# Optimization experiments

Hardware: AMD Instinct MI355X
Metric: run time of the kernel (lower is better)

## Reference

```python
import jax, jax.numpy as jnp
import numpy as np

B, L, D = 8, 4096, 1024
MAX_CHUNKS = 128
BOUNDARY_P = 0.03  # ~123 boundaries per sequence, just under max_chunks


def setup_inputs() -> dict:
    key = jax.random.key(0)
    kx, kb = jax.random.split(key)
    x = jax.random.normal(kx, (B, L, D), dtype=jnp.float32)
    # float 'boundary probabilities'; forward thresholds at 0.5 -> produce 0/1 floats
    boundaries = (jax.random.uniform(kb, (B, L)) < BOUNDARY_P).astype(jnp.float32)
    return {"x": x, "boundaries": boundaries}


def reference(x, boundaries):
    """Vectorized equivalent of ChunkLayer.forward.

    Chunk i of a sequence spans [b_i, b_{i+1}) for consecutive boundary
    positions (last chunk runs to seq end). Tokens before the first
    boundary get segment id -1 and are dropped, matching the torch loop.
    Output is mean-pooled chunks, zero-padded/truncated to MAX_CHUNKS.
    """
    Bb, Ll, Dd = x.shape
    bmask = (boundaries > 0.5).astype(jnp.int32)          # [B, L]
    seg = jnp.cumsum(bmask, axis=1) - 1                   # [B, L], -1 before first boundary
    # route dropped (seg<0) and overflow (seg>=MAX_CHUNKS) tokens to a trash segment
    seg = jnp.where((seg < 0) | (seg >= MAX_CHUNKS), MAX_CHUNKS, seg)

    def per_batch(xi, si):
        sums = jax.ops.segment_sum(xi, si, num_segments=MAX_CHUNKS + 1)[:MAX_CHUNKS]       # [C, D]
        cnts = jax.ops.segment_sum(jnp.ones((Ll,), xi.dtype), si,
                                   num_segments=MAX_CHUNKS + 1)[:MAX_CHUNKS]               # [C]
        return sums, cnts

    sums, cnts = jax.vmap(per_batch)(x, seg)              # [B, C, D], [B, C]
    means = jnp.where(cnts[..., None] > 0,
                      sums / jnp.maximum(cnts, 1.0)[..., None],
                      0.0)                                # zero-pad empty chunks
    return means, cnts.astype(jnp.int32)
```

## Files before the change

kernel.cpp:

```cpp
#include <hip/hip_runtime.h>

#define B_DIM 8
#define L_DIM 4096
#define D_DIM 1024
#define MAXC 128
#define RG 4
#define CT 256

__device__ __forceinline__ void f4add(float4& a, const float4& v) {
    a.x += v.x; a.y += v.y; a.z += v.z; a.w += v.w;
}

__global__ __launch_bounds__(1024, 8)
void fused_chunk_kernel(const float* __restrict__ x,
                        const float* __restrict__ bnd,
                        float* __restrict__ out_means,
                        float* __restrict__ out_cnts)
{
    const int bc   = blockIdx.x;
    const int b    = bc >> 7;
    const int c    = bc & (MAXC - 1);
    const int t    = threadIdx.x;
    const int tc   = t & (CT - 1);
    const int rg   = t >> 8;
    const int lane = t & 63;
    const int w    = t >> 6;

    __shared__ int wtot[16];
    __shared__ int sb[2];
    __shared__ float4 red[RG][CT];

    if (t == 0) { sb[0] = 0; sb[1] = L_DIM; }

    const float4 bv = reinterpret_cast<const float4*>(bnd + (size_t)b * L_DIM)[t];
    unsigned m = 0u;
    if (bv.x > 0.5f) m |= 1u;
    if (bv.y > 0.5f) m |= 2u;
    if (bv.z > 0.5f) m |= 4u;
    if (bv.w > 0.5f) m |= 8u;
    const int cnt4 = __popc(m);

    int incl = cnt4;
#pragma unroll
    for (int off = 1; off < 64; off <<= 1) {
        int u = __shfl_up(incl, off, 64);
        if (lane >= off) incl += u;
    }
    if (lane == 63) wtot[w] = incl;
    __syncthreads();

    int waveoff = 0, n = 0;
#pragma unroll
    for (int i = 0; i < 16; ++i) {
        const int ww = wtot[i];
        n += ww;
        if (i < w) waveoff += ww;
    }

    if (m != 0u) {
        int idx = waveoff + incl - cnt4;
        const int base = t * 4;
#pragma unroll
        for (int j = 0; j < 4; ++j) {
            if (m & (1u << j)) {
                if (idx == c)     sb[0] = base + j;
                if (idx == c + 1) sb[1] = base + j;
                ++idx;
            }
        }
    }
    __syncthreads();

    int cnt = 0;
    float4 a0 = make_float4(0.f, 0.f, 0.f, 0.f);
    float4 a1 = a0, a2 = a0, a3 = a0;

    if (c < n) {
        const int start = sb[0];
        const int end   = sb[1];
        cnt = end - start;

        const int nr = (cnt - rg + RG - 1) / RG;
        const float* xp = x + ((size_t)b * L_DIM + start + rg) * D_DIM + tc * 4;
        const size_t stride = (size_t)RG * D_DIM;

        int k = 0;
        for (; k + 8 <= nr; k += 8) {
            const float* base = xp + (size_t)k * stride;
            float4 v0 = *reinterpret_cast<const float4*>(base + 0 * stride);
            float4 v1 = *reinterpret_cast<const float4*>(base + 1 * stride);
            float4 v2 = *reinterpret_cast<const float4*>(base + 2 * stride);
            float4 v3 = *reinterpret_cast<const float4*>(base + 3 * stride);
            float4 v4 = *reinterpret_cast<const float4*>(base + 4 * stride);
            float4 v5 = *reinterpret_cast<const float4*>(base + 5 * stride);
            float4 v6 = *reinterpret_cast<const float4*>(base + 6 * stride);
            float4 v7 = *reinterpret_cast<const float4*>(base + 7 * stride);
            f4add(a0, v0); f4add(a1, v1); f4add(a2, v2); f4add(a3, v3);
            f4add(a0, v4); f4add(a1, v5); f4add(a2, v6); f4add(a3, v7);
        }
        if (k + 4 <= nr) {
            const float* base = xp + (size_t)k * stride;
            float4 v0 = *reinterpret_cast<const float4*>(base + 0 * stride);
            float4 v1 = *reinterpret_cast<const float4*>(base + 1 * stride);
            float4 v2 = *reinterpret_cast<const float4*>(base + 2 * stride);
            float4 v3 = *reinterpret_cast<const float4*>(base + 3 * stride);
            f4add(a0, v0); f4add(a1, v1); f4add(a2, v2); f4add(a3, v3);
            k += 4;
        }
        if (k + 2 <= nr) {
            const float* base = xp + (size_t)k * stride;
            float4 v0 = *reinterpret_cast<const float4*>(base + 0 * stride);
            float4 v1 = *reinterpret_cast<const float4*>(base + 1 * stride);
            f4add(a0, v0); f4add(a1, v1);
            k += 2;
        }
        if (k < nr) {
            f4add(a2, *reinterpret_cast<const float4*>(xp + (size_t)k * stride));
        }
        f4add(a0, a1); f4add(a2, a3);
        f4add(a0, a2);
    }

    red[rg][tc] = a0;
    __syncthreads();

    if (t < CT) {
        float4 s0 = red[0][t];
        f4add(s0, red[1][t]);
        f4add(s0, red[2][t]);
        f4add(s0, red[3][t]);
        const float inv = (cnt > 0) ? (1.0f / (float)cnt) : 0.0f;
        s0.x *= inv; s0.y *= inv; s0.z *= inv; s0.w *= inv;
        float4* op = reinterpret_cast<float4*>(out_means + (size_t)bc * D_DIM) + t;
        *op = s0;
        if (t == 0) out_cnts[bc] = (float)cnt;
    }
}

extern "C" void kernel_launch(void* const* d_in, const int* in_sizes, int n_in,
                              void* d_out, int out_size, void* d_ws, size_t ws_size,
                              hipStream_t stream)
{
    const float* x   = (const float*)d_in[0];
    const float* bnd = (const float*)d_in[1];

    float* out = (float*)d_out;
    float* out_means = out;
    float* out_cnts  = out + (size_t)B_DIM * MAXC * D_DIM;

    fused_chunk_kernel<<<B_DIM * MAXC, 1024, 0, stream>>>(x, bnd,
                                                          out_means, out_cnts);
}
```

Before: 31.65 us.

## Split each chunk's D dimension across four 256-thread blocks

Each (batch, chunk) pair is now handled by four blocks of 256 threads instead of one block of 1024, and each block covers a 256-column quarter of D. Within a block, a wave processes one row group and each lane loads a float4. Every thread now reads 16 boundary flags so the 4-wave scan still covers the full sequence. This gives four times as many smaller blocks, which may improve load balance and occupancy across CUs, at the cost of redoing the boundary scan four times per chunk.

```diff
diff --git a/kernel.cpp b/kernel.cpp
--- a/kernel.cpp
+++ b/kernel.cpp
@@ -5,63 +5,78 @@
 #define D_DIM 1024
 #define MAXC 128
 #define RG 4
-#define CT 256
+#define SC 64
 
 __device__ __forceinline__ void f4add(float4& a, const float4& v) {
     a.x += v.x; a.y += v.y; a.z += v.z; a.w += v.w;
 }
 
-__global__ __launch_bounds__(1024, 8)
+__global__ __launch_bounds__(256, 8)
 void fused_chunk_kernel(const float* __restrict__ x,
                         const float* __restrict__ bnd,
                         float* __restrict__ out_means,
                         float* __restrict__ out_cnts)
 {
-    const int bc   = blockIdx.x;
-    const int b    = bc >> 7;
-    const int c    = bc & (MAXC - 1);
+    const int gid  = blockIdx.x;
+    const int dq   = gid & 3;
+    const int bcC  = gid >> 2;
+    const int b    = bcC >> 7;
+    const int c    = bcC & (MAXC - 1);
     const int t    = threadIdx.x;
-    const int tc   = t & (CT - 1);
-    const int rg   = t >> 8;
     const int lane = t & 63;
-    const int w    = t >> 6;
+    const int wv   = t >> 6;
 
-    __shared__ int wtot[16];
+    __shared__ int wtot[RG];
     __shared__ int sb[2];
-    __shared__ float4 red[RG][CT];
+    __shared__ float4 red[RG][SC];
 
     if (t == 0) { sb[0] = 0; sb[1] = L_DIM; }
 
-    const float4 bv = reinterpret_cast<const float4*>(bnd + (size_t)b * L_DIM)[t];
     unsigned m = 0u;
-    if (bv.x > 0.5f) m |= 1u;
-    if (bv.y > 0.5f) m |= 2u;
-    if (bv.z > 0.5f) m |= 4u;
-    if (bv.w > 0.5f) m |= 8u;
-    const int cnt4 = __popc(m);
+    {
+        const float4* p4 = reinterpret_cast<const float4*>(bnd + (size_t)b * L_DIM) + t * 4;
+        float4 v0 = p4[0], v1 = p4[1], v2 = p4[2], v3 = p4[3];
+        if (v0.x > 0.5f) m |= 1u << 0;
+        if (v0.y > 0.5f) m |= 1u << 1;
+        if (v0.z > 0.5f) m |= 1u << 2;
+        if (v0.w > 0.5f) m |= 1u << 3;
+        if (v1.x > 0.5f) m |= 1u << 4;
+        if (v1.y > 0.5f) m |= 1u << 5;
+        if (v1.z > 0.5f) m |= 1u << 6;
+        if (v1.w > 0.5f) m |= 1u << 7;
+        if (v2.x > 0.5f) m |= 1u << 8;
+        if (v2.y > 0.5f) m |= 1u << 9;
+        if (v2.z > 0.5f) m |= 1u << 10;
+        if (v2.w > 0.5f) m |= 1u << 11;
+        if (v3.x > 0.5f) m |= 1u << 12;
+        if (v3.y > 0.5f) m |= 1u << 13;
+        if (v3.z > 0.5f) m |= 1u << 14;
+        if (v3.w > 0.5f) m |= 1u << 15;
+    }
+    const int cnt16 = __popc(m);
 
-    int incl = cnt4;
+    int incl = cnt16;
 #pragma unroll
     for (int off = 1; off < 64; off <<= 1) {
         int u = __shfl_up(incl, off, 64);
         if (lane >= off) incl += u;
     }
-    if (lane == 63) wtot[w] = incl;
+    if (lane == 63) wtot[wv] = incl;
     __syncthreads();
 
     int waveoff = 0, n = 0;
 #pragma unroll
-    for (int i = 0; i < 16; ++i) {
+    for (int i = 0; i < RG; ++i) {
         const int ww = wtot[i];
         n += ww;
-        if (i < w) waveoff += ww;
+        if (i < wv) waveoff += ww;
     }
 
     if (m != 0u) {
-        int idx = waveoff + incl - cnt4;
-        const int base = t * 4;
+        int idx = waveoff + incl - cnt16;
+        const int base = t * 16;
 #pragma unroll
-        for (int j = 0; j < 4; ++j) {
+        for (int j = 0; j < 16; ++j) {
             if (m & (1u << j)) {
                 if (idx == c)     sb[0] = base + j;
                 if (idx == c + 1) sb[1] = base + j;
@@ -80,8 +95,9 @@
         const int end   = sb[1];
         cnt = end - start;
 
-        const int nr = (cnt - rg + RG - 1) / RG;
-        const float* xp = x + ((size_t)b * L_DIM + start + rg) * D_DIM + tc * 4;
+        const int nr = (cnt - wv + RG - 1) / RG;
+        const float* xp = x + ((size_t)b * L_DIM + start + wv) * D_DIM
+                            + (size_t)(dq * SC + lane) * 4;
         const size_t stride = (size_t)RG * D_DIM;
 
         int k = 0;
@@ -121,19 +137,20 @@
         f4add(a0, a2);
     }
 
-    red[rg][tc] = a0;
+    red[wv][lane] = a0;
     __syncthreads();
 
-    if (t < CT) {
+    if (t < SC) {
         float4 s0 = red[0][t];
         f4add(s0, red[1][t]);
         f4add(s0, red[2][t]);
         f4add(s0, red[3][t]);
         const float inv = (cnt > 0) ? (1.0f / (float)cnt) : 0.0f;
         s0.x *= inv; s0.y *= inv; s0.z *= inv; s0.w *= inv;
-        float4* op = reinterpret_cast<float4*>(out_means + (size_t)bc * D_DIM) + t;
+        float4* op = reinterpret_cast<float4*>(out_means + (size_t)bcC * D_DIM)
+                     + dq * SC + t;
         *op = s0;
-        if (t == 0) out_cnts[bc] = (float)cnt;
+        if (t == 0 && dq == 0) out_cnts[bcC] = (float)cnt;
     }
 }
 
@@ -148,6 +165,6 @@
     float* out_means = out;
     float* out_cnts  = out + (size_t)B_DIM * MAXC * D_DIM;
 
-    fused_chunk_kernel<<<B_DIM * MAXC, 1024, 0, stream>>>(x, bnd,
-                                                          out_means, out_cnts);
+    fused_chunk_kernel<<<B_DIM * MAXC * 4, 256, 0, stream>>>(x, bnd,
+                                                             out_means, out_cnts);
 }
```

Result: faster. 29.00 us (-8.4%).
